# Kernel tuning notes

Hardware: AMD Instinct MI355X
Metric: run time of the kernel (lower is better)

The kernel has to match this reference:

```python
import jax, jax.numpy as jnp
import numpy as np

POOL = 7  # pool_size


def setup_inputs() -> dict:
    key = jax.random.key(0)
    k1, k2, k3, k4, k5 = jax.random.split(key, 5)
    H = W = 64
    C = 1024
    R = 1024  # num_rois
    img = jax.random.normal(k1, (1, H, W, C), dtype=jnp.float32)
    x = jax.random.randint(k2, (1, R), 0, W - 16)
    y = jax.random.randint(k3, (1, R), 0, H - 16)
    w = jax.random.randint(k4, (1, R), 1, 17)
    h = jax.random.randint(k5, (1, R), 1, 17)
    rois = jnp.stack([x, y, w, h], axis=-1).astype(jnp.int32)  # (1, R, 4)
    return {"img": img, "rois": rois}


def _axis_coords(start, size, pool):
    """Per-ROI bilinear source coords for tf.image.resize (half-pixel centers).
    start,size: (R,) int32. Returns absolute low/high indices (R,pool) int32
    and interpolation weight (R,pool) float32."""
    scale = size.astype(jnp.float32) / pool
    src = (jnp.arange(pool, dtype=jnp.float32) + 0.5)[None, :] * scale[:, None] - 0.5
    f = jnp.floor(src)
    lerp = src - f
    lo = jnp.clip(f.astype(jnp.int32), 0, size[:, None] - 1)
    hi = jnp.clip(f.astype(jnp.int32) + 1, 0, size[:, None] - 1)
    return start[:, None] + lo, start[:, None] + hi, lerp


def reference(img, rois):
    # img: (1, H, W, C); rois: (1, R, 4) int32 with (x, y, w, h)
    r = rois[0]
    x, y, w, h = r[:, 0], r[:, 1], r[:, 2], r[:, 3]
    y0, y1, ty = _axis_coords(y, h, POOL)  # (R, P)
    x0, x1, tx = _axis_coords(x, w, POOL)  # (R, P)
    im = img[0]  # (H, W, C)

    def gather(yy, xx):
        # (R, P, P, C) corner gather, vectorized over all ROIs
        return im[yy[:, :, None], xx[:, None, :], :]

    tx_ = tx[:, None, :, None]
    ty_ = ty[:, :, None, None]
    top = gather(y0, x0) * (1.0 - tx_) + gather(y0, x1) * tx_
    bot = gather(y1, x0) * (1.0 - tx_) + gather(y1, x1) * tx_
    out = top * (1.0 - ty_) + bot * ty_  # (R, P, P, C)
    return out[None]  # (1, R, P, P, C)
```

## Files before the change

kernel.cpp:

```cpp
#include <hip/hip_runtime.h>


#define POOLSZ 7
#define IMG_H 64
#define IMG_W 64
#define IMG_C 1024
#define NUM_XCD 8

typedef float v4f __attribute__((ext_vector_type(4)));

__global__ __launch_bounds__(256, 1) void roi_pool_row_kernel(
    const float* __restrict__ img,
    const int* __restrict__ rois,
    float* __restrict__ out,
    int roisPerXcd) {
    int r, py;
    if (roisPerXcd > 0) {
        const int xcd   = blockIdx.x & (NUM_XCD - 1);
        const int local = blockIdx.x >> 3;
        r  = xcd * roisPerXcd + local / POOLSZ;
        py = local % POOLSZ;
    } else {
        r  = blockIdx.x / POOLSZ;
        py = blockIdx.x % POOLSZ;
    }

    const int4 roi = ((const int4*)rois)[r];
    const int rx = roi.x, ry = roi.y, rw = roi.z, rh = roi.w;

    const float scy  = (float)rh * (1.0f / (float)POOLSZ);
    const float srcy = ((float)py + 0.5f) * scy - 0.5f;
    const float fy   = floorf(srcy);
    const float ty   = srcy - fy;
    const int   iy   = (int)fy;
    const int   y0   = ry + min(max(iy,     0), rh - 1);
    const int   y1   = ry + min(max(iy + 1, 0), rh - 1);

    int   x0[POOLSZ], x1[POOLSZ];
    float tx[POOLSZ];
    const float scx = (float)rw * (1.0f / (float)POOLSZ);
#pragma unroll
    for (int px = 0; px < POOLSZ; ++px) {
        const float srcx = ((float)px + 0.5f) * scx - 0.5f;
        const float fx   = floorf(srcx);
        tx[px] = srcx - fx;
        const int ix = (int)fx;
        x0[px] = rx + min(max(ix,     0), rw - 1);
        x1[px] = rx + min(max(ix + 1, 0), rw - 1);
    }

    const int c4 = threadIdx.x;
    const v4f* row0 = (const v4f*)(img + (size_t)y0 * IMG_W * IMG_C) + c4;
    const v4f* row1 = (const v4f*)(img + (size_t)y1 * IMG_W * IMG_C) + c4;

    v4f a[POOLSZ], b[POOLSZ], c[POOLSZ], d[POOLSZ];
#pragma unroll
    for (int px = 0; px < POOLSZ; ++px) {
        a[px] = row0[(size_t)x0[px] * (IMG_C / 4)];
        b[px] = row0[(size_t)x1[px] * (IMG_C / 4)];
        c[px] = row1[(size_t)x0[px] * (IMG_C / 4)];
        d[px] = row1[(size_t)x1[px] * (IMG_C / 4)];
    }

    v4f* dst = (v4f*)out + ((size_t)r * POOLSZ + py) * POOLSZ * (IMG_C / 4) + c4;
#pragma unroll
    for (int px = 0; px < POOLSZ; ++px) {
        const v4f top = a[px] + (b[px] - a[px]) * tx[px];
        const v4f bot = c[px] + (d[px] - c[px]) * tx[px];
        const v4f o   = top + (bot - top) * ty;
        dst[(size_t)px * (IMG_C / 4)] = o;
    }
}

extern "C" void kernel_launch(void* const* d_in, const int* in_sizes, int n_in,
                              void* d_out, int out_size, void* d_ws, size_t ws_size,
                              hipStream_t stream) {
    const float* img  = (const float*)d_in[0];
    const int*   rois = (const int*)d_in[1];
    float*       out  = (float*)d_out;
    const int R = in_sizes[1] / 4;
    const int n_rows = R * POOLSZ;
    const int roisPerXcd = (R % NUM_XCD == 0) ? (R / NUM_XCD) : 0;
    roi_pool_row_kernel<<<n_rows, 256, 0, stream>>>(img, rois, out, roisPerXcd);
}
```

Before: 236.1 us.

## Bucket-sort ROIs by y before pooling to improve per-XCD L2 locality

Adds a single-block kernel that counting-sorts ROI indices by their y coordinate into workspace. The pooling kernel then reads ROIs through this order, so the contiguous ROI chunk assigned to each XCD covers a narrower band of image rows, which should raise L2 hit rates on the gathered rows. The cost is an extra kernel launch, a serial one-block sort, and one indirect load per block. If the workspace is too small, the kernel falls back to the original order.

```diff
diff --git a/kernel.cpp b/kernel.cpp
--- a/kernel.cpp
+++ b/kernel.cpp
@@ -9,21 +9,47 @@
 
 typedef float v4f __attribute__((ext_vector_type(4)));
 
+__global__ __launch_bounds__(256) void roi_sort_kernel(
+    const int* __restrict__ rois, int* __restrict__ order, int R) {
+    __shared__ int cnt[64];
+    __shared__ int ofs[64];
+    const int t = threadIdx.x;
+    if (t < 64) cnt[t] = 0;
+    __syncthreads();
+    for (int r = t; r < R; r += 256) {
+        const int y = rois[r * 4 + 1] & 63;
+        atomicAdd(&cnt[y], 1);
+    }
+    __syncthreads();
+    if (t == 0) {
+        int s = 0;
+        for (int i = 0; i < 64; ++i) { ofs[i] = s; s += cnt[i]; }
+    }
+    __syncthreads();
+    for (int r = t; r < R; r += 256) {
+        const int y = rois[r * 4 + 1] & 63;
+        const int p = atomicAdd(&ofs[y], 1);
+        order[p] = r;
+    }
+}
+
 __global__ __launch_bounds__(256, 1) void roi_pool_row_kernel(
     const float* __restrict__ img,
     const int* __restrict__ rois,
     float* __restrict__ out,
-    int roisPerXcd) {
-    int r, py;
+    int roisPerXcd,
+    const int* __restrict__ order) {
+    int rIdx, py;
     if (roisPerXcd > 0) {
         const int xcd   = blockIdx.x & (NUM_XCD - 1);
         const int local = blockIdx.x >> 3;
-        r  = xcd * roisPerXcd + local / POOLSZ;
-        py = local % POOLSZ;
+        rIdx = xcd * roisPerXcd + local / POOLSZ;
+        py   = local % POOLSZ;
     } else {
-        r  = blockIdx.x / POOLSZ;
-        py = blockIdx.x % POOLSZ;
+        rIdx = blockIdx.x / POOLSZ;
+        py   = blockIdx.x % POOLSZ;
     }
+    const int r = order ? order[rIdx] : rIdx;
 
     const int4 roi = ((const int4*)rois)[r];
     const int rx = roi.x, ry = roi.y, rw = roi.z, rh = roi.w;
@@ -81,5 +107,11 @@
     const int R = in_sizes[1] / 4;
     const int n_rows = R * POOLSZ;
     const int roisPerXcd = (R % NUM_XCD == 0) ? (R / NUM_XCD) : 0;
-    roi_pool_row_kernel<<<n_rows, 256, 0, stream>>>(img, rois, out, roisPerXcd);
+
+    int* order = nullptr;
+    if (ws_size >= (size_t)R * sizeof(int)) {
+        order = (int*)d_ws;
+        roi_sort_kernel<<<1, 256, 0, stream>>>(rois, order, R);
+    }
+    roi_pool_row_kernel<<<n_rows, 256, 0, stream>>>(img, rois, out, roisPerXcd, order);
 }
```

New measurement: 233.1 us, median of 2. About the same (-1.3%).
